# Optimization experiments

Hardware: AMD Instinct MI355X
Metric: run time of the kernel (lower is better)

Reference implementation:

```python
import jax, jax.numpy as jnp
import numpy as np

N, K, F = 16384, 64, 2048
ALPHA = 1.0
GAMMA = 1.0


def setup_inputs() -> dict:
    key = jax.random.key(0)
    k1, k2, k3, k4 = jax.random.split(key, 4)
    features = jax.random.normal(k1, (N, F), dtype=jnp.float32)
    idx = jax.random.randint(k2, (N,), 0, K)
    labels = jax.nn.one_hot(idx, K, dtype=jnp.float32)  # [N, K] one-hot
    # original initializes clusters to zeros (degenerate); use small random values
    cluster = jax.random.normal(k3, (K, F), dtype=jnp.float32) * 0.02
    class_weight = jax.random.uniform(k4, (K,), dtype=jnp.float32, minval=0.5, maxval=1.5)
    return {"features": features, "labels": labels, "cluster": cluster,
            "class_weight": class_weight}


def reference(features, labels, cluster, class_weight):
    # ci: cluster center of each sample's argmax label  [N, F]
    idx = jnp.argmax(labels, axis=1)
    ci = cluster[idx]
    # numerator: squared distance to own center  [N]
    nume = jnp.sum((features - ci) ** 2, axis=1)
    # denom: sum_j ||c_j - c_i||^2 + alpha  (TF flattens cj to [N, K*F] and
    # tiles ci K times; the squared norm over that axis is exactly this sum)
    d2 = jnp.sum((cluster[:, None, :] - cluster[None, :, :]) ** 2, axis=-1)  # [K, K]
    row_sum = jnp.sum(d2, axis=1)                                            # [K]
    denom = row_sum[idx] + ALPHA                                             # [N]
    loss = (nume / denom)[:, None]                                           # [N, 1]
    # cluster update: weighted_delta[k,f] = sum_n cw[n,k]*labels[n,k]*(x[n,f]-c[k,f])/denom[n]
    # with cw[n,k] = labels[n,k] * class_weight[k]. Expressed without the
    # [N,K,F] intermediates the TF code materializes:
    A = (labels * labels) * class_weight[None, :] / denom[:, None]  # [N, K]
    weighted_delta = jnp.einsum('nk,nf->kf', A, features) - jnp.sum(A, axis=0)[:, None] * cluster
    new_cluster = cluster - GAMMA * weighted_delta  # assign_sub side effect
    return loss, new_cluster
```

## Files before the change

kernel.cpp:

```cpp
#include <hip/hip_runtime.h>

#define NROWS 16384
#define KC 64
#define FDIM 2048
#define F4 (FDIM / 4)
#define ALPHA 1.0f
#define GAMMA 1.0f
#define ROWS 16
#define HB 256
#define ROWS_PER_HB 64

typedef float f32x4 __attribute__((ext_vector_type(4)));

__global__ __launch_bounds__(256) void k_argmax_hist(
    const float* __restrict__ labels, int* __restrict__ idx,
    int* __restrict__ blockHist) {
    __shared__ int hist[KC];
    int t = threadIdx.x, w = t >> 6, lane = t & 63;
    if (t < KC) hist[t] = 0;
    __syncthreads();
    int rowbase = blockIdx.x * ROWS_PER_HB + w * 16;
    #pragma unroll
    for (int r0 = 0; r0 < 16; r0 += 4) {
        float v0 = labels[(rowbase + r0 + 0) * KC + lane];
        float v1 = labels[(rowbase + r0 + 1) * KC + lane];
        float v2 = labels[(rowbase + r0 + 2) * KC + lane];
        float v3 = labels[(rowbase + r0 + 3) * KC + lane];
        unsigned long long m0 = __ballot(v0 > 0.5f);
        unsigned long long m1 = __ballot(v1 > 0.5f);
        unsigned long long m2 = __ballot(v2 > 0.5f);
        unsigned long long m3 = __ballot(v3 > 0.5f);
        if (lane == 0) {
            int k0 = __ffsll(m0) - 1;
            int k1 = __ffsll(m1) - 1;
            int k2 = __ffsll(m2) - 1;
            int k3 = __ffsll(m3) - 1;
            idx[rowbase + r0 + 0] = k0;
            idx[rowbase + r0 + 1] = k1;
            idx[rowbase + r0 + 2] = k2;
            idx[rowbase + r0 + 3] = k3;
            atomicAdd(&hist[k0], 1);
            atomicAdd(&hist[k1], 1);
            atomicAdd(&hist[k2], 1);
            atomicAdd(&hist[k3], 1);
        }
    }
    __syncthreads();
    if (t < KC) blockHist[blockIdx.x * KC + t] = hist[t];
}

__global__ __launch_bounds__(256) void k_prefix(
    const int* __restrict__ blockHist, int* __restrict__ blockBase,
    int* __restrict__ counts, int* __restrict__ offsets) {
    int t = threadIdx.x;
    int c = t >> 6;
    int k = t & 63;
    __shared__ int chunkTot[4][KC];
    __shared__ int kTot[KC];
    int acc = 0;
    for (int b = c * 64; b < c * 64 + 64; ++b) acc += blockHist[b * KC + k];
    chunkTot[c][k] = acc;
    __syncthreads();
    if (c == 0) {
        int tot = chunkTot[0][k] + chunkTot[1][k] + chunkTot[2][k] + chunkTot[3][k];
        kTot[k] = tot;
        counts[k] = tot;
    }
    __syncthreads();
    if (t == 0) {
        int a = 0;
        for (int j = 0; j < KC; ++j) { offsets[j] = a; a += kTot[j]; }
    }
    int run = 0;
    for (int cc = 0; cc < c; ++cc) run += chunkTot[cc][k];
    for (int b = c * 64; b < c * 64 + 64; ++b) {
        blockBase[b * KC + k] = run;
        run += blockHist[b * KC + k];
    }
}

__global__ __launch_bounds__(64) void k_scatter(
    const int* __restrict__ idx, const int* __restrict__ offsets,
    const int* __restrict__ blockBase, int* __restrict__ order) {
    __shared__ int cur[KC];
    int t = threadIdx.x;
    cur[t] = offsets[t] + blockBase[blockIdx.x * KC + t];
    __syncthreads();
    int n = blockIdx.x * ROWS_PER_HB + t;
    int k = idx[n];
    int p = atomicAdd(&cur[k], 1);
    order[p] = n;
}

__global__ __launch_bounds__(256) void k_rowsum(
    const float* __restrict__ cluster, const float* __restrict__ cw,
    float* __restrict__ inv_denom, float* __restrict__ scale) {
    int k = blockIdx.x, t = threadIdx.x;
    const float4* c4 = (const float4*)cluster;
    float4 a0 = c4[k * F4 + t];
    float4 a1 = c4[k * F4 + 256 + t];
    float acc = 0.f;
    for (int j = 0; j < KC; ++j) {
        float4 b0 = c4[j * F4 + t];
        float4 b1 = c4[j * F4 + 256 + t];
        float d;
        d = a0.x - b0.x; acc += d * d;
        d = a0.y - b0.y; acc += d * d;
        d = a0.z - b0.z; acc += d * d;
        d = a0.w - b0.w; acc += d * d;
        d = a1.x - b1.x; acc += d * d;
        d = a1.y - b1.y; acc += d * d;
        d = a1.z - b1.z; acc += d * d;
        d = a1.w - b1.w; acc += d * d;
    }
    #pragma unroll
    for (int off = 32; off >= 1; off >>= 1) acc += __shfl_down(acc, off);
    __shared__ float red[4];
    if ((t & 63) == 0) red[t >> 6] = acc;
    __syncthreads();
    if (t == 0) {
        float denom = red[0] + red[1] + red[2] + red[3] + ALPHA;
        inv_denom[k] = 1.0f / denom;
        scale[k]     = cw[k] / denom;
    }
}

__global__ __launch_bounds__(256) void k_main(
    const float* __restrict__ features, const float* __restrict__ cluster,
    const int* __restrict__ idx, const int* __restrict__ order,
    const float* __restrict__ inv_denom, float* __restrict__ delta,
    float* __restrict__ loss) {
    int t = threadIdx.x;
    int pair = blockIdx.x >> 1, half = blockIdx.x & 1;
    int foff = half * 256;
    __shared__ float part[ROWS][256];
    __shared__ int onum[ROWS];
    __shared__ int okk[ROWS];
    if (t < ROWS) {
        int n = order[pair * ROWS + t];
        onum[t] = n;
        okk[t]  = idx[n];
    }
    __syncthreads();

    const f32x4* f4 = (const f32x4*)features;
    const f32x4* c4 = (const f32x4*)cluster;
    float4 s = {0.f, 0.f, 0.f, 0.f};
    int k0 = okk[0];

    if (okk[ROWS - 1] == k0) {
        f32x4 cv = c4[k0 * F4 + foff + t];
        for (int r = 0; r < ROWS; r += 4) {
            f32x4 x0 = __builtin_nontemporal_load(&f4[(size_t)onum[r + 0] * F4 + foff + t]);
            f32x4 x1 = __builtin_nontemporal_load(&f4[(size_t)onum[r + 1] * F4 + foff + t]);
            f32x4 x2 = __builtin_nontemporal_load(&f4[(size_t)onum[r + 2] * F4 + foff + t]);
            f32x4 x3 = __builtin_nontemporal_load(&f4[(size_t)onum[r + 3] * F4 + foff + t]);
            float d, p;
            s.x += x0.x; s.y += x0.y; s.z += x0.z; s.w += x0.w;
            p = 0.f;
            d = x0.x - cv.x; p += d * d;
            d = x0.y - cv.y; p += d * d;
            d = x0.z - cv.z; p += d * d;
            d = x0.w - cv.w; p += d * d;
            part[r + 0][t] = p;
            s.x += x1.x; s.y += x1.y; s.z += x1.z; s.w += x1.w;
            p = 0.f;
            d = x1.x - cv.x; p += d * d;
            d = x1.y - cv.y; p += d * d;
            d = x1.z - cv.z; p += d * d;
            d = x1.w - cv.w; p += d * d;
            part[r + 1][t] = p;
            s.x += x2.x; s.y += x2.y; s.z += x2.z; s.w += x2.w;
            p = 0.f;
            d = x2.x - cv.x; p += d * d;
            d = x2.y - cv.y; p += d * d;
            d = x2.z - cv.z; p += d * d;
            d = x2.w - cv.w; p += d * d;
            part[r + 2][t] = p;
            s.x += x3.x; s.y += x3.y; s.z += x3.z; s.w += x3.w;
            p = 0.f;
            d = x3.x - cv.x; p += d * d;
            d = x3.y - cv.y; p += d * d;
            d = x3.z - cv.z; p += d * d;
            d = x3.w - cv.w; p += d * d;
            part[r + 3][t] = p;
        }
        float* dk = delta + k0 * FDIM + half * 1024;
        atomicAdd(&dk[t * 4 + 0], s.x);
        atomicAdd(&dk[t * 4 + 1], s.y);
        atomicAdd(&dk[t * 4 + 2], s.z);
        atomicAdd(&dk[t * 4 + 3], s.w);
    } else {
        int cur_k = -1;
        f32x4 cv;
        for (int r = 0; r < ROWS; ++r) {
            int k = okk[r];
            if (k != cur_k) {
                if (cur_k >= 0) {
                    float* dk = delta + cur_k * FDIM + half * 1024;
                    atomicAdd(&dk[t * 4 + 0], s.x);
                    atomicAdd(&dk[t * 4 + 1], s.y);
                    atomicAdd(&dk[t * 4 + 2], s.z);
                    atomicAdd(&dk[t * 4 + 3], s.w);
                    s.x = s.y = s.z = s.w = 0.f;
                }
                cv = c4[k * F4 + foff + t];
                cur_k = k;
            }
            f32x4 x = __builtin_nontemporal_load(&f4[(size_t)onum[r] * F4 + foff + t]);
            s.x += x.x; s.y += x.y; s.z += x.z; s.w += x.w;
            float d, p = 0.f;
            d = x.x - cv.x; p += d * d;
            d = x.y - cv.y; p += d * d;
            d = x.z - cv.z; p += d * d;
            d = x.w - cv.w; p += d * d;
            part[r][t] = p;
        }
        float* dk = delta + cur_k * FDIM + half * 1024;
        atomicAdd(&dk[t * 4 + 0], s.x);
        atomicAdd(&dk[t * 4 + 1], s.y);
        atomicAdd(&dk[t * 4 + 2], s.z);
        atomicAdd(&dk[t * 4 + 3], s.w);
    }
    __syncthreads();
    int w = t >> 6, l = t & 63;
    for (int r = w; r < ROWS; r += 4) {
        float v = part[r][l] + part[r][l + 64] + part[r][l + 128] + part[r][l + 192];
        #pragma unroll
        for (int off = 32; off >= 1; off >>= 1) v += __shfl_down(v, off);
        if (l == 0) {
            atomicAdd(&loss[onum[r]], v * inv_denom[okk[r]]);
        }
    }
}

__global__ __launch_bounds__(256) void k_finalize(
    const float* __restrict__ cluster, const float* __restrict__ delta,
    const int* __restrict__ counts, const float* __restrict__ scale,
    float* __restrict__ outc) {
    int e = blockIdx.x * 256 + threadIdx.x;
    int k = e >> 9;
    const float4* c4 = (const float4*)cluster;
    const float4* d4 = (const float4*)delta;
    float4 c = c4[e], d = d4[e];
    float s = scale[k], cnt = (float)counts[k];
    float4 o;
    o.x = c.x - GAMMA * s * (d.x - cnt * c.x);
    o.y = c.y - GAMMA * s * (d.y - cnt * c.y);
    o.z = c.z - GAMMA * s * (d.z - cnt * c.z);
    o.w = c.w - GAMMA * s * (d.w - cnt * c.w);
    ((float4*)outc)[e] = o;
}

extern "C" void kernel_launch(void* const* d_in, const int* in_sizes, int n_in,
                              void* d_out, int out_size, void* d_ws, size_t ws_size,
                              hipStream_t stream) {
    const float* features = (const float*)d_in[0];
    const float* labels   = (const float*)d_in[1];
    const float* cluster  = (const float*)d_in[2];
    const float* cw       = (const float*)d_in[3];
    float* loss = (float*)d_out;
    float* outc = (float*)d_out + NROWS;

    char*  ws        = (char*)d_ws;
    float* delta     = (float*)ws;
    int*   counts    = (int*)(ws + (size_t)KC * FDIM * 4);
    int*   offsets   = counts + KC;
    float* inv_denom = (float*)(offsets + KC);
    float* scale     = inv_denom + KC;
    int*   idx       = (int*)(scale + KC);
    int*   order     = idx + NROWS;
    int*   blockHist = order + NROWS;
    int*   blockBase = blockHist + HB * KC;

    hipMemsetAsync(delta, 0, (size_t)KC * FDIM * 4, stream);
    hipMemsetAsync(loss, 0, (size_t)NROWS * 4, stream);

    k_argmax_hist<<<HB, 256, 0, stream>>>(labels, idx, blockHist);
    k_rowsum<<<KC, 256, 0, stream>>>(cluster, cw, inv_denom, scale);
    k_prefix<<<1, 256, 0, stream>>>(blockHist, blockBase, counts, offsets);
    k_scatter<<<HB, 64, 0, stream>>>(idx, offsets, blockBase, order);
    k_main<<<(NROWS / ROWS) * 2, 256, 0, stream>>>(features, cluster, idx, order,
                                                   inv_denom, delta, loss);
    k_finalize<<<(KC * F4) / 256, 256, 0, stream>>>(cluster, delta, counts, scale, outc);
}
```

Measured before the change: 237.8 us.

## Fold memsets and small kernels together to cut launch count

Removes both hipMemsetAsync calls: delta is now zeroed inside the histogram kernel, and loss is written as two per-half partials that the finalize kernel sums. The prefix-scan and cluster row-sum kernels are merged into one launch, and the histogram is rebuilt with 128 blocks of 128 rows. The aim is to cut launch and memset overhead on a pipeline of small kernels. In exchange it adds a lossPart workspace buffer and a few extra blocks in finalize.

Result: faster. 225.2 us, median of 2 (-5.3%).

```diff
diff --git a/kernel.cpp b/kernel.cpp
--- a/kernel.cpp
+++ b/kernel.cpp
@@ -7,21 +7,23 @@
 #define ALPHA 1.0f
 #define GAMMA 1.0f
 #define ROWS 16
-#define HB 256
-#define ROWS_PER_HB 64
+#define HB 128
+#define ROWS_PER_HB 128
 
 typedef float f32x4 __attribute__((ext_vector_type(4)));
 
 __global__ __launch_bounds__(256) void k_argmax_hist(
     const float* __restrict__ labels, int* __restrict__ idx,
-    int* __restrict__ blockHist) {
+    int* __restrict__ blockHist, float4* __restrict__ delta4) {
     __shared__ int hist[KC];
     int t = threadIdx.x, w = t >> 6, lane = t & 63;
     if (t < KC) hist[t] = 0;
-    __syncthreads();
-    int rowbase = blockIdx.x * ROWS_PER_HB + w * 16;
+    float4 z = {0.f, 0.f, 0.f, 0.f};
+    delta4[blockIdx.x * 256 + t] = z;
+    __syncthreads();
+    int rowbase = blockIdx.x * ROWS_PER_HB + w * 32;
     #pragma unroll
-    for (int r0 = 0; r0 < 16; r0 += 4) {
+    for (int r0 = 0; r0 < 32; r0 += 4) {
         float v0 = labels[(rowbase + r0 + 0) * KC + lane];
         float v1 = labels[(rowbase + r0 + 1) * KC + lane];
         float v2 = labels[(rowbase + r0 + 2) * KC + lane];
@@ -49,42 +51,73 @@
     if (t < KC) blockHist[blockIdx.x * KC + t] = hist[t];
 }
 
-__global__ __launch_bounds__(256) void k_prefix(
+__global__ __launch_bounds__(256) void k_prefix_rowsum(
     const int* __restrict__ blockHist, int* __restrict__ blockBase,
-    int* __restrict__ counts, int* __restrict__ offsets) {
-    int t = threadIdx.x;
-    int c = t >> 6;
-    int k = t & 63;
-    __shared__ int chunkTot[4][KC];
-    __shared__ int kTot[KC];
-    int acc = 0;
-    for (int b = c * 64; b < c * 64 + 64; ++b) acc += blockHist[b * KC + k];
-    chunkTot[c][k] = acc;
-    __syncthreads();
-    if (c == 0) {
-        int tot = chunkTot[0][k] + chunkTot[1][k] + chunkTot[2][k] + chunkTot[3][k];
-        kTot[k] = tot;
-        counts[k] = tot;
-    }
-    __syncthreads();
-    if (t == 0) {
-        int a = 0;
-        for (int j = 0; j < KC; ++j) { offsets[j] = a; a += kTot[j]; }
-    }
-    int run = 0;
-    for (int cc = 0; cc < c; ++cc) run += chunkTot[cc][k];
-    for (int b = c * 64; b < c * 64 + 64; ++b) {
-        blockBase[b * KC + k] = run;
-        run += blockHist[b * KC + k];
-    }
-}
-
-__global__ __launch_bounds__(64) void k_scatter(
+    int* __restrict__ counts, int* __restrict__ offsets,
+    const float* __restrict__ cluster, const float* __restrict__ cw,
+    float* __restrict__ inv_denom, float* __restrict__ scale) {
+    if (blockIdx.x == 0) {
+        int t = threadIdx.x, c = t >> 6, k = t & 63;
+        __shared__ int chunkTot[4][KC];
+        __shared__ int kTot[KC];
+        int acc = 0;
+        for (int b = c * 32; b < c * 32 + 32; ++b) acc += blockHist[b * KC + k];
+        chunkTot[c][k] = acc;
+        __syncthreads();
+        if (c == 0) {
+            int tot = chunkTot[0][k] + chunkTot[1][k] + chunkTot[2][k] + chunkTot[3][k];
+            kTot[k] = tot;
+            counts[k] = tot;
+        }
+        __syncthreads();
+        if (t == 0) {
+            int a = 0;
+            for (int j = 0; j < KC; ++j) { offsets[j] = a; a += kTot[j]; }
+        }
+        int run = 0;
+        for (int cc = 0; cc < c; ++cc) run += chunkTot[cc][k];
+        for (int b = c * 32; b < c * 32 + 32; ++b) {
+            blockBase[b * KC + k] = run;
+            run += blockHist[b * KC + k];
+        }
+    } else {
+        int k = blockIdx.x - 1, t = threadIdx.x;
+        const float4* c4 = (const float4*)cluster;
+        float4 a0 = c4[k * F4 + t];
+        float4 a1 = c4[k * F4 + 256 + t];
+        float acc = 0.f;
+        for (int j = 0; j < KC; ++j) {
+            float4 b0 = c4[j * F4 + t];
+            float4 b1 = c4[j * F4 + 256 + t];
+            float d;
+            d = a0.x - b0.x; acc += d * d;
+            d = a0.y - b0.y; acc += d * d;
+            d = a0.z - b0.z; acc += d * d;
+            d = a0.w - b0.w; acc += d * d;
+            d = a1.x - b1.x; acc += d * d;
+            d = a1.y - b1.y; acc += d * d;
+            d = a1.z - b1.z; acc += d * d;
+            d = a1.w - b1.w; acc += d * d;
+        }
+        #pragma unroll
+        for (int off = 32; off >= 1; off >>= 1) acc += __shfl_down(acc, off);
+        __shared__ float red[4];
+        if ((t & 63) == 0) red[t >> 6] = acc;
+        __syncthreads();
+        if (t == 0) {
+            float denom = red[0] + red[1] + red[2] + red[3] + ALPHA;
+            inv_denom[k] = 1.0f / denom;
+            scale[k]     = cw[k] / denom;
+        }
+    }
+}
+
+__global__ __launch_bounds__(128) void k_scatter(
     const int* __restrict__ idx, const int* __restrict__ offsets,
     const int* __restrict__ blockBase, int* __restrict__ order) {
     __shared__ int cur[KC];
     int t = threadIdx.x;
-    cur[t] = offsets[t] + blockBase[blockIdx.x * KC + t];
+    if (t < KC) cur[t] = offsets[t] + blockBase[blockIdx.x * KC + t];
     __syncthreads();
     int n = blockIdx.x * ROWS_PER_HB + t;
     int k = idx[n];
@@ -92,44 +125,11 @@
     order[p] = n;
 }
 
-__global__ __launch_bounds__(256) void k_rowsum(
-    const float* __restrict__ cluster, const float* __restrict__ cw,
-    float* __restrict__ inv_denom, float* __restrict__ scale) {
-    int k = blockIdx.x, t = threadIdx.x;
-    const float4* c4 = (const float4*)cluster;
-    float4 a0 = c4[k * F4 + t];
-    float4 a1 = c4[k * F4 + 256 + t];
-    float acc = 0.f;
-    for (int j = 0; j < KC; ++j) {
-        float4 b0 = c4[j * F4 + t];
-        float4 b1 = c4[j * F4 + 256 + t];
-        float d;
-        d = a0.x - b0.x; acc += d * d;
-        d = a0.y - b0.y; acc += d * d;
-        d = a0.z - b0.z; acc += d * d;
-        d = a0.w - b0.w; acc += d * d;
-        d = a1.x - b1.x; acc += d * d;
-        d = a1.y - b1.y; acc += d * d;
-        d = a1.z - b1.z; acc += d * d;
-        d = a1.w - b1.w; acc += d * d;
-    }
-    #pragma unroll
-    for (int off = 32; off >= 1; off >>= 1) acc += __shfl_down(acc, off);
-    __shared__ float red[4];
-    if ((t & 63) == 0) red[t >> 6] = acc;
-    __syncthreads();
-    if (t == 0) {
-        float denom = red[0] + red[1] + red[2] + red[3] + ALPHA;
-        inv_denom[k] = 1.0f / denom;
-        scale[k]     = cw[k] / denom;
-    }
-}
-
 __global__ __launch_bounds__(256) void k_main(
     const float* __restrict__ features, const float* __restrict__ cluster,
     const int* __restrict__ idx, const int* __restrict__ order,
     const float* __restrict__ inv_denom, float* __restrict__ delta,
-    float* __restrict__ loss) {
+    float* __restrict__ lossPart) {
     int t = threadIdx.x;
     int pair = blockIdx.x >> 1, half = blockIdx.x & 1;
     int foff = half * 256;
@@ -229,7 +229,7 @@
         #pragma unroll
         for (int off = 32; off >= 1; off >>= 1) v += __shfl_down(v, off);
         if (l == 0) {
-            atomicAdd(&loss[onum[r]], v * inv_denom[okk[r]]);
+            lossPart[half * NROWS + onum[r]] = v * inv_denom[okk[r]];
         }
     }
 }
@@ -237,19 +237,26 @@
 __global__ __launch_bounds__(256) void k_finalize(
     const float* __restrict__ cluster, const float* __restrict__ delta,
     const int* __restrict__ counts, const float* __restrict__ scale,
-    float* __restrict__ outc) {
-    int e = blockIdx.x * 256 + threadIdx.x;
-    int k = e >> 9;
-    const float4* c4 = (const float4*)cluster;
-    const float4* d4 = (const float4*)delta;
-    float4 c = c4[e], d = d4[e];
-    float s = scale[k], cnt = (float)counts[k];
-    float4 o;
-    o.x = c.x - GAMMA * s * (d.x - cnt * c.x);
-    o.y = c.y - GAMMA * s * (d.y - cnt * c.y);
-    o.z = c.z - GAMMA * s * (d.z - cnt * c.z);
-    o.w = c.w - GAMMA * s * (d.w - cnt * c.w);
-    ((float4*)outc)[e] = o;
+    const float* __restrict__ lossPart, float* __restrict__ outc,
+    float* __restrict__ loss) {
+    int b = blockIdx.x, t = threadIdx.x;
+    if (b < 128) {
+        int e = b * 256 + t;
+        int k = e >> 9;
+        const float4* c4 = (const float4*)cluster;
+        const float4* d4 = (const float4*)delta;
+        float4 c = c4[e], d = d4[e];
+        float s = scale[k], cnt = (float)counts[k];
+        float4 o;
+        o.x = c.x - GAMMA * s * (d.x - cnt * c.x);
+        o.y = c.y - GAMMA * s * (d.y - cnt * c.y);
+        o.z = c.z - GAMMA * s * (d.z - cnt * c.z);
+        o.w = c.w - GAMMA * s * (d.w - cnt * c.w);
+        ((float4*)outc)[e] = o;
+    } else {
+        int n = (b - 128) * 256 + t;
+        loss[n] = lossPart[n] + lossPart[NROWS + n];
+    }
 }
 
 extern "C" void kernel_launch(void* const* d_in, const int* in_sizes, int n_in,
@@ -272,15 +279,14 @@
     int*   order     = idx + NROWS;
     int*   blockHist = order + NROWS;
     int*   blockBase = blockHist + HB * KC;
-
-    hipMemsetAsync(delta, 0, (size_t)KC * FDIM * 4, stream);
-    hipMemsetAsync(loss, 0, (size_t)NROWS * 4, stream);
-
-    k_argmax_hist<<<HB, 256, 0, stream>>>(labels, idx, blockHist);
-    k_rowsum<<<KC, 256, 0, stream>>>(cluster, cw, inv_denom, scale);
-    k_prefix<<<1, 256, 0, stream>>>(blockHist, blockBase, counts, offsets);
-    k_scatter<<<HB, 64, 0, stream>>>(idx, offsets, blockBase, order);
+    float* lossPart  = (float*)(blockBase + HB * KC);
+
+    k_argmax_hist<<<HB, 256, 0, stream>>>(labels, idx, blockHist, (float4*)delta);
+    k_prefix_rowsum<<<KC + 1, 256, 0, stream>>>(blockHist, blockBase, counts, offsets,
+                                                cluster, cw, inv_denom, scale);
+    k_scatter<<<HB, 128, 0, stream>>>(idx, offsets, blockBase, order);
     k_main<<<(NROWS / ROWS) * 2, 256, 0, stream>>>(features, cluster, idx, order,
-                                                   inv_denom, delta, loss);
-    k_finalize<<<(KC * F4) / 256, 256, 0, stream>>>(cluster, delta, counts, scale, outc);
-}
+                                                   inv_denom, delta, lossPart);
+    k_finalize<<<192, 256, 0, stream>>>(cluster, delta, counts, scale, lossPart,
+                                        outc, loss);
+}
```
